# Kernel tuning notes

Hardware: AMD Instinct MI355X
Metric: run time of the kernel (lower is better)

Reference implementation:

```python
import jax, jax.numpy as jnp
import numpy as np
import math

D_MODEL = 512
NUM_CLASSES = 8
MEM_SLOTS = 64
STEPS = 4
DECAY = 0.9
TOPK = 8
SCORE_CLIP = 10.0
VOCAB = 32000
MAX_LEN = 2048
B, T = 32, 2048


def _linear_params(key, d_in, d_out):
    kw, kb = jax.random.split(key)
    W = jax.random.normal(kw, (d_in, d_out), jnp.float32) * (1.0 / math.sqrt(d_in))
    b = jnp.zeros((d_out,), jnp.float32)
    return W, b


def setup_inputs() -> dict:
    key = jax.random.key(0)
    ks = jax.random.split(key, 16)
    inp = {}
    inp["input_ids"] = jax.random.randint(ks[0], (B, T), 0, VOCAB)
    inp["attention_mask"] = jnp.ones((B, T), jnp.int32)
    inp["token_emb"] = jax.random.normal(ks[1], (VOCAB, D_MODEL), jnp.float32) * 0.02
    inp["pos_emb"] = jax.random.normal(ks[2], (MAX_LEN, D_MODEL), jnp.float32) * 0.02
    inp["memory_init"] = jax.random.normal(ks[3], (1, MEM_SLOTS, D_MODEL), jnp.float32) * 0.02
    names = ["q", "k", "v", "write", "gate", "rq", "rk", "rv"]
    for i, n in enumerate(names):
        W, b = _linear_params(ks[4 + i], D_MODEL, D_MODEL)
        inp[n + "_W"], inp[n + "_b"] = W, b
    inp["fuse_W"], inp["fuse_b"] = _linear_params(ks[12], 2 * D_MODEL, D_MODEL)
    inp["cls_W"], inp["cls_b"] = _linear_params(ks[13], D_MODEL, NUM_CLASSES)
    inp["tln_g"] = jnp.ones((D_MODEL,), jnp.float32)
    inp["tln_b"] = jnp.zeros((D_MODEL,), jnp.float32)
    inp["mln_g"] = jnp.ones((D_MODEL,), jnp.float32)
    inp["mln_b"] = jnp.zeros((D_MODEL,), jnp.float32)
    return inp


def _layer_norm(x, g, b, eps=1e-5):
    mu = jnp.mean(x, axis=-1, keepdims=True)
    var = jnp.var(x, axis=-1, keepdims=True)
    return (x - mu) * jax.lax.rsqrt(var + eps) * g + b


def _topk_softmax(scores, k):
    # scores: (B, T, S). Equivalent to scatter top-k vals into -inf then softmax:
    # softmax over the top-k entries, zeros elsewhere.
    Bb, Tt, S = scores.shape
    tv, ti = jax.lax.top_k(scores, k)           # (B,T,k)
    w = jax.nn.softmax(tv, axis=-1)
    rows = jnp.arange(Bb * Tt)[:, None]
    out = jnp.zeros((Bb * Tt, S), scores.dtype).at[rows, ti.reshape(-1, k)].set(w.reshape(-1, k))
    return out.reshape(Bb, Tt, S)


def _binding(scores, mask_f, k):
    w = _topk_softmax(jnp.clip(scores, -SCORE_CLIP, SCORE_CLIP), k)
    w = w * mask_f
    return w / jnp.maximum(jnp.sum(w, axis=-1, keepdims=True), 1e-9)


def _forward(input_ids, attention_mask, token_emb, pos_emb, memory_init,
             q_W, q_b, k_W, k_b, v_W, v_b, write_W, write_b, gate_W, gate_b,
             rq_W, rq_b, rk_W, rk_b, rv_W, rv_b, fuse_W, fuse_b,
             cls_W, cls_b, tln_g, tln_b, mln_g, mln_b):
    scale = 1.0 / math.sqrt(D_MODEL)
    tokens = token_emb[input_ids] + pos_emb[jnp.arange(input_ids.shape[1])][None]
    tokens = _layer_norm(tokens, tln_g, tln_b)  # (B,T,D)
    mask_f = attention_mask[..., None].astype(tokens.dtype)  # (B,T,1)
    memory = jnp.broadcast_to(memory_init, (input_ids.shape[0], MEM_SLOTS, D_MODEL))
    for _ in range(STEPS):
        q = tokens @ q_W + q_b
        kk = memory @ k_W + k_b
        scores = jnp.einsum("btd,bsd->bts", q, kk) * scale
        binding = _binding(scores, mask_f, TOPK)  # (B,T,S)
        v = tokens @ v_W + v_b
        write = jnp.einsum("bts,btd->bsd", binding, v)
        slot_usage = jnp.maximum(jnp.sum(binding, axis=1)[..., None], 1e-6)  # (B,S,1)
        write = (write / slot_usage) @ write_W + write_b
        write = jax.nn.sigmoid(write @ gate_W + gate_b) * write
        memory = _layer_norm(DECAY * memory + (1.0 - DECAY) * write, mln_g, mln_b)
    # read
    rq = tokens @ rq_W + rq_b
    rk = memory @ rk_W + rk_b
    rv = memory @ rv_W + rv_b
    scores = jnp.einsum("btd,bsd->bts", rq, rk) * scale
    rw = _binding(scores, mask_f, TOPK)
    context = jnp.einsum("bts,bsd->btd", rw, rv)
    fused = jnp.concatenate([tokens, context], axis=-1) @ fuse_W + fuse_b
    pooled = jnp.sum(fused * mask_f, axis=1) / jnp.maximum(jnp.sum(mask_f, axis=1), 1.0)
    return pooled @ cls_W + cls_b  # (B, C)


def reference(input_ids, attention_mask, token_emb, pos_emb, memory_init,
              q_W, q_b, k_W, k_b, v_W, v_b, write_W, write_b, gate_W, gate_b,
              rq_W, rq_b, rk_W, rk_b, rv_W, rv_b, fuse_W, fuse_b,
              cls_W, cls_b, tln_g, tln_b, mln_g, mln_b):
    return _forward(input_ids, attention_mask, token_emb, pos_emb, memory_init,
                    q_W, q_b, k_W, k_b, v_W, v_b, write_W, write_b, gate_W, gate_b,
                    rq_W, rq_b, rk_W, rk_b, rv_W, rv_b, fuse_W, fuse_b,
                    cls_W, cls_b, tln_g, tln_b, mln_g, mln_b)
```

## Files before the change

kernel.cpp:

```cpp
#include <hip/hip_runtime.h>
#include <hip/hip_bf16.h>
#include <math.h>

#define BB 32
#define TT 2048
#define DM 512
#define SS 64
#define BT (BB*TT)
#define NSTEPS 4
#define SCALE 0.044194173824159216f

typedef unsigned short u16;
typedef unsigned int u32;
typedef __attribute__((ext_vector_type(8))) short s16x8;
typedef __attribute__((ext_vector_type(4))) float f32x4;
typedef __attribute__((ext_vector_type(4))) unsigned u32x4;

__device__ __forceinline__ u16 f2b(float x){
  __hip_bfloat16 h = __float2bfloat16(x);
  return *reinterpret_cast<u16*>(&h);
}
__device__ __forceinline__ float b2f(u16 u){
  __hip_bfloat16 h;
  *reinterpret_cast<u16*>(&h) = u;
  return __bfloat162float(h);
}

static __device__ __forceinline__ float wave_reduce_sum(float v){
  #pragma unroll
  for (int off=32; off; off>>=1) v += __shfl_down(v, off);
  return v;
}

__global__ __launch_bounds__(256) void embed_ln_k(const int* __restrict__ ids,
    const float* __restrict__ temb, const float* __restrict__ pemb,
    const float* __restrict__ g, const float* __restrict__ be, u16* __restrict__ out){
  int row = blockIdx.x*4 + (threadIdx.x>>6);
  int l = threadIdx.x & 63;
  int t = row & (TT-1);
  int id = ids[row];
  const float* te = temb + (size_t)id*DM + l*8;
  const float* pe = pemb + (size_t)t*DM + l*8;
  float4 a0 = *(const float4*)te,     a1 = *(const float4*)(te+4);
  float4 p0 = *(const float4*)pe,     p1 = *(const float4*)(pe+4);
  float x[8] = {a0.x+p0.x, a0.y+p0.y, a0.z+p0.z, a0.w+p0.w,
                a1.x+p1.x, a1.y+p1.y, a1.z+p1.z, a1.w+p1.w};
  float s1 = 0.f, s2 = 0.f;
  #pragma unroll
  for (int e=0;e<8;e++){ s1 += x[e]; s2 += x[e]*x[e]; }
  #pragma unroll
  for (int off=1; off<64; off<<=1){ s1 += __shfl_xor(s1, off); s2 += __shfl_xor(s2, off); }
  float mu = s1*(1.f/DM);
  float var = s2*(1.f/DM) - mu*mu;
  float rs = rsqrtf(var + 1e-5f);
  const float* gp = g + l*8;
  const float* bp = be + l*8;
  float4 g0=*(const float4*)gp, g1=*(const float4*)(gp+4);
  float4 b0=*(const float4*)bp, b1=*(const float4*)(bp+4);
  float gg[8]={g0.x,g0.y,g0.z,g0.w,g1.x,g1.y,g1.z,g1.w};
  float bb[8]={b0.x,b0.y,b0.z,b0.w,b1.x,b1.y,b1.z,b1.w};
  s16x8 o;
  #pragma unroll
  for (int e=0;e<8;e++) o[e] = (short)f2b((x[e]-mu)*rs*gg[e] + bb[e]);
  *(s16x8*)(out + (size_t)row*DM + l*8) = o;
}

template<int EPI>
__global__ __launch_bounds__(128) void ntgemm_k(const u16* __restrict__ A,
    const u16* __restrict__ Bm, const float* __restrict__ bias,
    const u16* __restrict__ mulb, const float* __restrict__ rowv,
    const float* __restrict__ bias2, void* __restrict__ Cout, float scalep){
  int m0 = blockIdx.x*32 + (threadIdx.x>>6)*16;
  int n0 = blockIdx.y*64;
  int l = threadIdx.x & 63;
  int lr = l & 15, lk = (l>>4)*8;
  const u16* Arow = A + (size_t)(m0 + lr)*512 + lk;
  const u16* B0   = Bm + (size_t)(n0 + lr)*512 + lk;
  f32x4 acc[4] = {};
  #pragma unroll
  for (int k0=0;k0<512;k0+=32){
    s16x8 a = *(const s16x8*)(Arow + k0);
    #pragma unroll
    for (int j=0;j<4;j++){
      s16x8 b = *(const s16x8*)(B0 + (size_t)j*16*512 + k0);
      acc[j] = __builtin_amdgcn_mfma_f32_16x16x32_bf16(a, b, acc[j], 0,0,0);
    }
  }
  int mbase = m0 + (l>>4)*4;
  #pragma unroll
  for (int j=0;j<4;j++){
    int n = n0 + j*16 + lr;
    #pragma unroll
    for (int r=0;r<4;r++){
      int m = mbase + r;
      float v = acc[j][r];
      if (EPI==2){
        float z = v + bias[n];
        float sg = 1.f/(1.f + expf(-z));
        ((float*)Cout)[(size_t)m*512 + n] = b2f(mulb[(size_t)m*512 + n]) * sg;
      }
      if (EPI==3){ ((float*)Cout)[(size_t)m*512 + n] = v + bias[n]; }
      if (EPI==5){ ((u16*)Cout)[(size_t)m*512 + n] = f2b(v + rowv[m]*bias[n] + bias2[n]); }
    }
  }
}

__global__ __launch_bounds__(128) void ptcb_k(const u16* __restrict__ A,
    const u16* __restrict__ Bm, const float* __restrict__ bias,
    const float* __restrict__ mem, const float* __restrict__ wcb,
    const float* __restrict__ cb0p, u16* __restrict__ Pt, float* __restrict__ cb){
  int l = threadIdx.x & 63;
  if (blockIdx.y < 8){
    int m0 = blockIdx.x*32 + (threadIdx.x>>6)*16;
    int n0 = blockIdx.y*64;
    int lr = l & 15, lk = (l>>4)*8;
    const u16* Arow = A + (size_t)(m0 + lr)*512 + lk;
    const u16* B0   = Bm + (size_t)(n0 + lr)*512 + lk;
    f32x4 acc[4] = {};
    #pragma unroll
    for (int k0=0;k0<512;k0+=32){
      s16x8 a = *(const s16x8*)(Arow + k0);
      #pragma unroll
      for (int j=0;j<4;j++){
        s16x8 b = *(const s16x8*)(B0 + (size_t)j*16*512 + k0);
        acc[j] = __builtin_amdgcn_mfma_f32_16x16x32_bf16(a, b, acc[j], 0,0,0);
      }
    }
    int mbase = m0 + (l>>4)*4;
    #pragma unroll
    for (int j=0;j<4;j++){
      int n = n0 + j*16 + lr;
      #pragma unroll
      for (int r=0;r<4;r++)
        Pt[(size_t)(mbase+r)*512 + n] = f2b(acc[j][r] + bias[n]);
    }
  } else {
    int base = blockIdx.x*32 + (threadIdx.x>>6)*16;
    for (int i=0;i<16;i++){
      int row = base + i;
      const float* r = mem + (size_t)row*512;
      float s = 0.f;
      #pragma unroll
      for (int k=0;k<8;k++) s += r[l + 64*k]*wcb[l + 64*k];
      #pragma unroll
      for (int off=32; off; off>>=1) s += __shfl_xor(s, off);
      if (l==0) cb[row] = s + cb0p[0];
    }
  }
}

__global__ __launch_bounds__(64) void bind_k(const u16* __restrict__ tok,
    const u16* __restrict__ Pt, const float* __restrict__ cbuf, const int* __restrict__ mask,
    u16* __restrict__ BNDT, float* __restrict__ cspart){
  int b = blockIdx.y, t0 = blockIdx.x*64;
  int l = threadIdx.x;
  int lr = l&15, g = l>>4, lk = g*8;
  __shared__ float sc[64*66];
  __shared__ u16 bt[64*66];

  const u16* Abase = tok + ((size_t)(b*TT + t0 + lr))*512 + lk;
  const u16* Bbase = Pt + ((size_t)(b*SS + lr))*512 + lk;
  f32x4 acc[4][4] = {};
  #pragma unroll
  for (int k0=0;k0<512;k0+=32){
    s16x8 a[4], bb[4];
    #pragma unroll
    for (int mi=0;mi<4;mi++) a[mi] = *(const s16x8*)(Abase + (size_t)mi*16*512 + k0);
    #pragma unroll
    for (int nj=0;nj<4;nj++) bb[nj] = *(const s16x8*)(Bbase + (size_t)nj*16*512 + k0);
    #pragma unroll
    for (int mi=0;mi<4;mi++)
      #pragma unroll
      for (int nj=0;nj<4;nj++)
        acc[mi][nj] = __builtin_amdgcn_mfma_f32_16x16x32_bf16(a[mi], bb[nj], acc[mi][nj], 0,0,0);
  }
  float cbv[4];
  #pragma unroll
  for (int nj=0;nj<4;nj++) cbv[nj] = cbuf[b*SS + 16*nj + lr];
  #pragma unroll
  for (int mi=0;mi<4;mi++)
    #pragma unroll
    for (int nj=0;nj<4;nj++)
      #pragma unroll
      for (int r=0;r<4;r++){
        float x = acc[mi][nj][r] + cbv[nj];
        x = fminf(fmaxf(x, -10.f), 10.f);
        sc[(16*mi + 4*g + r)*66 + 16*nj + lr] = x;
      }

  float sv[64];
  #pragma unroll
  for (int j=0;j<64;j++) sv[j] = sc[l*66 + j];

  u32 work[64];
  #pragma unroll
  for (int j=0;j<64;j++){
    u32 s = __float_as_uint(sv[j]);
    u32 o = s ^ ((u32)(((int)s) >> 31) | 0x80000000u);
    work[j] = (o & 0xFFFFFFC0u) | (u32)(63 - j);
  }
  u32 mtop = 0;
  #pragma unroll
  for (int it=0; it<8; ++it){
    u32 a[32];
    #pragma unroll
    for (int j=0;j<32;j++){ u32 x = work[2*j], y = work[2*j+1]; a[j] = x>y?x:y; }
    #pragma unroll
    for (int lvl=16; lvl>=1; lvl>>=1)
      #pragma unroll
      for (int j=0;j<lvl;j++){ u32 x = a[2*j], y = a[2*j+1]; a[j] = x>y?x:y; }
    u32 m = a[0];
    if (it==0) mtop = m;
    #pragma unroll
    for (int j=0;j<64;j++) work[j] = (work[j]==m) ? 0u : work[j];
  }
  u32 ot = mtop & 0xFFFFFFC0u;
  u32 tb = (ot & 0x80000000u) ? (ot ^ 0x80000000u) : ~ot;
  float T = __uint_as_float(tb);

  float tot = 0.f;
  #pragma unroll
  for (int j=0;j<64;j++){
    float ej = (work[j]==0u) ? expf(sv[j]-T) : 0.f;
    sv[j] = ej;
    tot += ej;
  }
  int mv = mask[b*TT + t0 + l];
  float inv = mv ? 1.f/tot : 0.f;
  #pragma unroll
  for (int j=0;j<64;j++)
    bt[j*66 + l] = f2b(sv[j]*inv);

  const u32* btw = (const u32*)bt;
  u32 rowbuf[32];
  float csum = 0.f;
  #pragma unroll
  for (int w=0;w<32;w++){
    u32 v = btw[l*33 + w];
    rowbuf[w] = v;
    csum += b2f((u16)(v & 0xFFFFu)) + b2f((u16)(v >> 16));
  }
  cspart[((size_t)b*32 + blockIdx.x)*64 + l] = csum;
  u16* dst = BNDT + ((size_t)(b*SS + l))*TT + t0;
  #pragma unroll
  for (int w8=0;w8<8;w8++){
    u32x4 v;
    v[0]=rowbuf[4*w8]; v[1]=rowbuf[4*w8+1]; v[2]=rowbuf[4*w8+2]; v[3]=rowbuf[4*w8+3];
    *(u32x4*)(dst + 8*w8) = v;
  }
}

__global__ __launch_bounds__(64) void csred_k(const float* __restrict__ cspart,
    float* __restrict__ slot, float* __restrict__ rr, float* __restrict__ raw){
  int b = blockIdx.x, s = threadIdx.x;
  float t = 0.f;
  for (int k=0;k<32;k++) t += cspart[((size_t)b*32 + k)*64 + s];
  raw[b*SS+s] = t;
  float sl = fmaxf(t, 1e-6f);
  slot[b*SS+s] = sl;
  rr[b*SS+s] = t/sl;
}

__global__ __launch_bounds__(256) void wtfused_k(const u16* __restrict__ BNDT,
    const u16* __restrict__ tok, const float* __restrict__ slot, u16* __restrict__ t1h){
  int dgrp = blockIdx.x, b = blockIdx.y;
  int tid = threadIdx.x, w = tid>>6, l = tid&63;
  int lr = l&15, lk = (l>>4)*8;
  __shared__ u16 tk[64][72];
  f32x4 acc[4] = {};
  int trow = tid>>2, dcol = (tid&3)*16;
  const u16* tokbase = tok + ((size_t)b*TT)*512 + dgrp*64;
  const u16* Abase = BNDT + ((size_t)(b*SS + 16*w + lr))*TT;
  for (int tb=0; tb<TT; tb+=64){
    const u16* src = tokbase + (size_t)(tb + trow)*512 + dcol;
    s16x8 v0 = *(const s16x8*)(src);
    s16x8 v1 = *(const s16x8*)(src+8);
    #pragma unroll
    for (int e=0;e<8;e++){
      int d0 = dcol+e, d1 = dcol+8+e;
      tk[d0][(trow + 8*((d0>>5)&1)) & 63] = (u16)v0[e];
      tk[d1][(trow + 8*((d1>>5)&1)) & 63] = (u16)v1[e];
    }
    __syncthreads();
    #pragma unroll
    for (int kst=0;kst<2;kst++){
      s16x8 a = *(const s16x8*)(Abase + tb + kst*32 + lk);
      #pragma unroll
      for (int nt=0;nt<4;nt++){
        int dd = nt*16 + lr;
        int cb2 = (kst*32 + lk + 8*((dd>>5)&1)) & 63;
        s16x8 bb = *(const s16x8*)&tk[dd][cb2];
        acc[nt] = __builtin_amdgcn_mfma_f32_16x16x32_bf16(a, bb, acc[nt], 0,0,0);
      }
    }
    __syncthreads();
  }
  #pragma unroll
  for (int nt=0;nt<4;nt++){
    int d = dgrp*64 + nt*16 + lr;
    #pragma unroll
    for (int r=0;r<4;r++){
      int s = 16*w + (l>>4)*4 + r;
      int row = b*64 + s;
      t1h[(size_t)row*512 + d] = f2b(acc[nt][r] / slot[row]);
    }
  }
}

__global__ __launch_bounds__(256) void allconv_k(
    const float* __restrict__ s0, u16* __restrict__ d0,
    const float* __restrict__ s1, u16* __restrict__ d1,
    const float* __restrict__ s2, u16* __restrict__ d2,
    const float* __restrict__ s3, u16* __restrict__ d3,
    const float* __restrict__ s4, u16* __restrict__ d4){
  int sel = blockIdx.x >> 10;
  int i = (blockIdx.x & 1023)*256 + threadIdx.x;
  const float* s; u16* d;
  if (sel==0){s=s0;d=d0;} else if (sel==1){s=s1;d=d1;} else if (sel==2){s=s2;d=d2;}
  else if (sel==3){s=s3;d=d3;} else {s=s4;d=d4;}
  d[i] = f2b(s[i]);
}

__global__ __launch_bounds__(256) void alltconv_k(
    const float* __restrict__ s0, u16* __restrict__ d0,
    const float* __restrict__ s1, u16* __restrict__ d1,
    const float* __restrict__ s2, u16* __restrict__ d2){
  const float* in; u16* out;
  if (blockIdx.z==0){in=s0;out=d0;} else if (blockIdx.z==1){in=s1;out=d1;} else {in=s2;out=d2;}
  __shared__ float t[32][33];
  int c0 = blockIdx.x*32, r0 = blockIdx.y*32;
  int cx = threadIdx.x&31, ry = threadIdx.x>>5;
  #pragma unroll
  for (int i=0;i<4;i++){ int r = ry + i*8; t[r][cx] = in[(size_t)(r0+r)*512 + c0+cx]; }
  __syncthreads();
  #pragma unroll
  for (int i=0;i<4;i++){ int r = ry + i*8; out[(size_t)(c0+r)*512 + r0+cx] = f2b(t[cx][r]); }
}

__global__ __launch_bounds__(128) void pregemm_k(
    const u16* __restrict__ A0, const u16* __restrict__ B0, u16* __restrict__ C0, float p0,
    const u16* __restrict__ A1, const u16* __restrict__ B1, u16* __restrict__ C1, float p1,
    const u16* __restrict__ A2, const u16* __restrict__ B2, u16* __restrict__ C2, float p2){
  const u16* A; const u16* Bm; u16* C; float sp;
  if (blockIdx.z==0){A=A0;Bm=B0;C=C0;sp=p0;}
  else if (blockIdx.z==1){A=A1;Bm=B1;C=C1;sp=p1;}
  else {A=A2;Bm=B2;C=C2;sp=p2;}
  int m0 = blockIdx.x*32 + (threadIdx.x>>6)*16;
  int n0 = blockIdx.y*64;
  int l = threadIdx.x & 63;
  int lr = l & 15, lk = (l>>4)*8;
  const u16* Arow = A + (size_t)(m0 + lr)*512 + lk;
  const u16* Bp   = Bm + (size_t)(n0 + lr)*512 + lk;
  f32x4 acc[4] = {};
  #pragma unroll
  for (int k0=0;k0<512;k0+=32){
    s16x8 a = *(const s16x8*)(Arow + k0);
    #pragma unroll
    for (int j=0;j<4;j++){
      s16x8 b = *(const s16x8*)(Bp + (size_t)j*16*512 + k0);
      acc[j] = __builtin_amdgcn_mfma_f32_16x16x32_bf16(a, b, acc[j], 0,0,0);
    }
  }
  int mbase = m0 + (l>>4)*4;
  #pragma unroll
  for (int j=0;j<4;j++){
    int n = n0 + j*16 + lr;
    #pragma unroll
    for (int r=0;r<4;r++)
      C[(size_t)(mbase+r)*512 + n] = f2b(acc[j][r] * sp);
  }
}

__global__ __launch_bounds__(256) void smalls_k(
    const float* __restrict__ qW, const float* __restrict__ kB, float* __restrict__ bq,
    const float* __restrict__ rqW, const float* __restrict__ rkB, float* __restrict__ bq_r,
    const float* __restrict__ kW, const float* __restrict__ qB, float* __restrict__ wcb,
    const float* __restrict__ rkW, const float* __restrict__ rqB, float* __restrict__ wcb_r,
    const float* __restrict__ wrW, const float* __restrict__ vB, float* __restrict__ bvw,
    float* __restrict__ cb0s){
  int blk = blockIdx.x;
  if (blk < 512){
    int which = blk >> 7;
    const float* W; const float* v; float* out;
    if (which==0){W=qW; v=kB; out=bq;}
    else if (which==1){W=rqW; v=rkB; out=bq_r;}
    else if (which==2){W=kW; v=qB; out=wcb;}
    else {W=rkW; v=rqB; out=wcb_r;}
    int i = (blk&127)*4 + (threadIdx.x>>6), l = threadIdx.x&63;
    const float* r = W + (size_t)i*512;
    float s = 0.f;
    #pragma unroll
    for (int k=0;k<8;k++) s += r[l + 64*k]*v[l + 64*k];
    #pragma unroll
    for (int off=32; off; off>>=1) s += __shfl_xor(s, off);
    if (l==0) out[i] = s * SCALE;
  } else if (blk < 514){
    int n = (blk-512)*256 + threadIdx.x;
    float s = 0.f;
    for (int o=0;o<512;o++) s += vB[o]*wrW[(size_t)o*512 + n];
    bvw[n] = s;
  } else {
    if (threadIdx.x < 128){
      int w = threadIdx.x>>6, l = threadIdx.x&63;
      const float* a = w ? rkB : kB;
      const float* bvec = w ? rqB : qB;
      float s = 0.f;
      #pragma unroll
      for (int k=0;k<8;k++) s += a[l + 64*k]*bvec[l + 64*k];
      #pragma unroll
      for (int off=32; off; off>>=1) s += __shfl_xor(s, off);
      if (l==0) cb0s[w] = s * SCALE;
    }
  }
}

__global__ __launch_bounds__(256) void meminit_k(const float* __restrict__ src,
    float* __restrict__ mem, u16* __restrict__ memh){
  int i = blockIdx.x*256 + threadIdx.x;
  float v = src[i & (SS*DM-1)];
  mem[i] = v;
  memh[i] = f2b(v);
}

__global__ __launch_bounds__(256) void mem_ln_k(float* __restrict__ mem, const float* __restrict__ w3,
    const float* __restrict__ g, const float* __restrict__ be, u16* __restrict__ memh){
  int row = blockIdx.x;
  int d = threadIdx.x;
  float* mrow = mem + (size_t)row*DM;
  const float* wrow = w3 + (size_t)row*DM;
  float x0 = 0.9f*mrow[d]     + 0.1f*wrow[d];
  float x1 = 0.9f*mrow[d+256] + 0.1f*wrow[d+256];
  float s1 = x0+x1, s2 = x0*x0 + x1*x1;
  s1 = wave_reduce_sum(s1); s2 = wave_reduce_sum(s2);
  __shared__ float r1[4], r2[4];
  int lane = d & 63, w = d>>6;
  if (lane==0){ r1[w]=s1; r2[w]=s2; }
  __syncthreads();
  float S1 = r1[0]+r1[1]+r1[2]+r1[3];
  float S2 = r2[0]+r2[1]+r2[2]+r2[3];
  float mu = S1 * (1.f/DM);
  float var = S2*(1.f/DM) - mu*mu;
  float rs = rsqrtf(var + 1e-5f);
  float y0 = (x0-mu)*rs*g[d] + be[d];
  float y1 = (x1-mu)*rs*g[d+256] + be[d+256];
  mrow[d] = y0; mrow[d+256] = y1;
  memh[(size_t)row*DM + d] = f2b(y0);
  memh[(size_t)row*DM + d+256] = f2b(y1);
}

__global__ __launch_bounds__(256) void tokpart_k(const u16* __restrict__ tok,
    const int* __restrict__ mask, float* __restrict__ tp){
  int b = blockIdx.x, sl = blockIdx.y;
  int w = threadIdx.x>>6, l = threadIdx.x&63;
  float acc[8] = {};
  #pragma unroll 4
  for (int i=0;i<32;i++){
    int t = sl*128 + w + 4*i;
    float m = (float)mask[b*TT + t];
    s16x8 v = *(const s16x8*)(tok + ((size_t)(b*TT + t))*512 + l*8);
    #pragma unroll
    for (int e=0;e<8;e++) acc[e] += m*b2f((u16)v[e]);
  }
  float* dst = tp + ((size_t)(b*64 + sl*4 + w))*512 + l*8;
  #pragma unroll
  for (int e=0;e<8;e++) dst[e] = acc[e];
}

__global__ __launch_bounds__(256) void catden_k(const float* __restrict__ tp,
    const float* __restrict__ rws, const float* __restrict__ rv,
    const int* __restrict__ mask, float* __restrict__ cat, float* __restrict__ denomv){
  int b = blockIdx.x, tid = threadIdx.x;
  float dn = 0.f;
  for (int t=tid; t<TT; t+=256) dn += (float)mask[b*TT+t];
  dn = wave_reduce_sum(dn);
  __shared__ float dred[4];
  if ((tid&63)==0) dred[tid>>6]=dn;
  #pragma unroll
  for (int it=0; it<2; ++it){
    int d = tid + it*256;
    float ts = 0.f;
    for (int k=0;k<64;k++) ts += tp[((size_t)(b*64+k))*512 + d];
    cat[(size_t)b*1024 + d] = ts;
    float c = 0.f;
    for (int s=0;s<SS;s++) c += rws[b*SS+s]*rv[((size_t)b*SS+s)*DM + d];
    cat[(size_t)b*1024 + 512 + d] = c;
  }
  __syncthreads();
  if (tid==0) denomv[b] = dred[0]+dred[1]+dred[2]+dred[3];
}

__global__ __launch_bounds__(256) void fuse_k(const float* __restrict__ cat,
    const float* __restrict__ denomv, const float* __restrict__ fuseW,
    const float* __restrict__ fuseb, float* __restrict__ pooled){
  int b = blockIdx.x, n0 = blockIdx.y*64;
  int l = threadIdx.x&63, kc = threadIdx.x>>6;
  int n = n0 + l;
  float acc = 0.f;
  const float* crow = cat + (size_t)b*1024;
  for (int k=kc*256; k<kc*256+256; ++k)
    acc += crow[k]*fuseW[(size_t)k*512 + n];
  __shared__ float red[4][64];
  red[kc][l] = acc;
  __syncthreads();
  if (kc==0){
    float denom = denomv[b];
    float tot = red[0][l]+red[1][l]+red[2][l]+red[3][l];
    pooled[(size_t)b*512 + n] = (tot + denom*fuseb[n]) / fmaxf(denom, 1.f);
  }
}

__global__ __launch_bounds__(256) void cls_k(const float* __restrict__ pooled,
    const float* __restrict__ clsW, const float* __restrict__ clsb, float* __restrict__ out){
  int b = blockIdx.x;
  int c = threadIdx.x&7, kc = threadIdx.x>>3;
  float acc = 0.f;
  const float* prow = pooled + (size_t)b*512;
  for (int d=kc*16; d<kc*16+16; ++d) acc += prow[d]*clsW[d*8+c];
  __shared__ float red[32][8];
  red[kc][c] = acc;
  __syncthreads();
  if (threadIdx.x < 8){
    float tot = 0.f;
    #pragma unroll
    for (int k=0;k<32;k++) tot += red[k][threadIdx.x];
    out[b*8 + threadIdx.x] = tot + clsb[threadIdx.x];
  }
}

extern "C" void kernel_launch(void* const* d_in, const int* in_sizes, int n_in,
                              void* d_out, int out_size, void* d_ws, size_t ws_size,
                              hipStream_t stream){
  (void)in_sizes; (void)n_in; (void)out_size; (void)ws_size;
  const int*   ids   = (const int*)d_in[0];
  const int*   amask = (const int*)d_in[1];
  const float* temb  = (const float*)d_in[2];
  const float* pemb  = (const float*)d_in[3];
  const float* mem0  = (const float*)d_in[4];
  const float* qW=(const float*)d_in[5],  *qB=(const float*)d_in[6];
  const float* kW=(const float*)d_in[7],  *kB=(const float*)d_in[8];
  const float* vW=(const float*)d_in[9],  *vB=(const float*)d_in[10];
  const float* wrW=(const float*)d_in[11],*wrB=(const float*)d_in[12];
  const float* gtW=(const float*)d_in[13],*gtB=(const float*)d_in[14];
  const float* rqW=(const float*)d_in[15],*rqB=(const float*)d_in[16];
  const float* rkW=(const float*)d_in[17],*rkB=(const float*)d_in[18];
  const float* rvW=(const float*)d_in[19],*rvB=(const float*)d_in[20];
  const float* fW=(const float*)d_in[21], *fB=(const float*)d_in[22];
  const float* cW=(const float*)d_in[23], *cB=(const float*)d_in[24];
  const float* tg=(const float*)d_in[25], *tb=(const float*)d_in[26];
  const float* mg=(const float*)d_in[27], *mb=(const float*)d_in[28];

  char* p = (char*)d_ws;
  size_t off = 0;
  auto alloc = [&](size_t bytes)->char*{ char* r = p + off; off += (bytes + 255) & ~(size_t)255; return r; };
  u16*   tokens = (u16*)  alloc((size_t)BT*DM*2);
  u16*   Pt     = (u16*)  alloc((size_t)BB*SS*DM*2);
  u16*   BNDT   = (u16*)  alloc((size_t)BB*SS*TT*2);
  float* cspart = (float*)alloc((size_t)BB*32*64*4);
  float* scratch= (float*)alloc((size_t)4*2048*512*4);
  u16*   t1h    = (u16*)  alloc((size_t)2048*512*2);
  u16*   zh     = (u16*)  alloc((size_t)2048*512*2);
  float* mem    = (float*)alloc((size_t)BB*SS*DM*4);
  u16*   memh   = (u16*)  alloc((size_t)BB*SS*DM*2);
  u16*   wrWT   = (u16*)  alloc(512*512*2);
  u16*   gtWT   = (u16*)  alloc(512*512*2);
  u16*   rvWT   = (u16*)  alloc(512*512*2);
  u16*   WqkT   = (u16*)  alloc(512*512*2);
  u16*   WqkT_r = (u16*)  alloc(512*512*2);
  u16*   WvwT   = (u16*)  alloc(512*512*2);
  float* bq     = (float*)alloc(512*4);
  float* bq_r   = (float*)alloc(512*4);
  float* wcb    = (float*)alloc(512*4);
  float* wcb_r  = (float*)alloc(512*4);
  float* bvw    = (float*)alloc(512*4);
  float* cb0s   = (float*)alloc(256);
  float* cbuf   = (float*)alloc(2048*4);
  float* slot   = (float*)alloc(2048*4);
  float* rr     = (float*)alloc(2048*4);
  float* raw    = (float*)alloc(2048*4);
  float* catbuf = (float*)alloc((size_t)BB*1024*4);
  float* denomv = (float*)alloc(BB*4);
  float* pooled = (float*)alloc((size_t)BB*512*4);
  float* rv32   = scratch;
  float* tspart = scratch + 1048576;
  float* gh32   = scratch + 2097152;
  u16*   qWb    = (u16*)((char*)scratch + 12582912);
  u16*   kWb    = qWb + 512*512;
  u16*   rqWb   = kWb + 512*512;
  u16*   rkWb   = rqWb + 512*512;
  u16*   vWb    = (u16*)((char*)scratch + 14680064);

  allconv_k<<<5120, 256, 0, stream>>>(qW, qWb, kW, kWb, rqW, rqWb, rkW, rkWb, vW, vWb);
  alltconv_k<<<dim3(16,16,3), 256, 0, stream>>>(wrW, wrWT, gtW, gtWT, rvW, rvWT);
  pregemm_k<<<dim3(16,8,3), 128, 0, stream>>>(qWb, kWb, WqkT, SCALE,
                                              rqWb, rkWb, WqkT_r, SCALE,
                                              wrWT, vWb, WvwT, 1.0f);
  smalls_k<<<515, 256, 0, stream>>>(qW, kB, bq, rqW, rkB, bq_r, kW, qB, wcb,
                                    rkW, rqB, wcb_r, wrW, vB, bvw, cb0s);
  embed_ln_k<<<BT/4, 256, 0, stream>>>(ids, temb, pemb, tg, tb, tokens);
  meminit_k<<<(BB*SS*DM)/256, 256, 0, stream>>>(mem0, mem, memh);

  for (int step=0; step<NSTEPS; ++step){
    ptcb_k<<<dim3(64,9), 128, 0, stream>>>(memh, WqkT, bq, mem, wcb, cb0s, Pt, cbuf);
    bind_k<<<dim3(32,32), 64, 0, stream>>>(tokens, Pt, cbuf, amask, BNDT, cspart);
    csred_k<<<32, 64, 0, stream>>>(cspart, slot, rr, raw);
    wtfused_k<<<dim3(8,32), 256, 0, stream>>>(BNDT, tokens, slot, t1h);
    ntgemm_k<5><<<dim3(64,8), 128, 0, stream>>>(t1h, WvwT, bvw, nullptr, rr, wrB, zh, 0.f);
    ntgemm_k<2><<<dim3(64,8), 128, 0, stream>>>(zh, gtWT, gtB, zh, nullptr, nullptr, gh32, 0.f);
    mem_ln_k<<<BB*SS, 256, 0, stream>>>(mem, gh32, mg, mb, memh);
  }

  ptcb_k<<<dim3(64,9), 128, 0, stream>>>(memh, WqkT_r, bq_r, mem, wcb_r, cb0s+1, Pt, cbuf);
  bind_k<<<dim3(32,32), 64, 0, stream>>>(tokens, Pt, cbuf, amask, BNDT, cspart);
  csred_k<<<32, 64, 0, stream>>>(cspart, slot, rr, raw);
  ntgemm_k<3><<<dim3(64,8), 128, 0, stream>>>(memh, rvWT, rvB, nullptr, nullptr, nullptr, rv32, 0.f);
  tokpart_k<<<dim3(32,16), 256, 0, stream>>>(tokens, amask, tspart);
  catden_k<<<32, 256, 0, stream>>>(tspart, raw, rv32, amask, catbuf, denomv);
  fuse_k<<<dim3(32,8), 256, 0, stream>>>(catbuf, denomv, fW, fB, pooled);
  cls_k<<<32, 256, 0, stream>>>(pooled, cW, cB, (float*)d_out);
}
```

Measured before the change: 624.5 us.

## Split-K the binding-weighted token GEMM and process two rows per wave in embed LN

The memory-write GEMM (binding^T × tokens) is split along T into 4 partitions, each block covering 128 output columns. Partial fp32 sums go to a scratch buffer, and a separate reduction kernel adds them and applies the slot normalization. This raises the block count from 256 to 512 and halves the token reads per output column, which helps occupancy on a GPU with many CUs. The cost is extra fp32 partial-sum traffic and one more launch per step. Separately, embed_ln now handles two rows per wave to raise memory-level parallelism.

```diff
diff --git a/kernel.cpp b/kernel.cpp
--- a/kernel.cpp
+++ b/kernel.cpp
@@ -35,34 +35,48 @@
 __global__ __launch_bounds__(256) void embed_ln_k(const int* __restrict__ ids,
     const float* __restrict__ temb, const float* __restrict__ pemb,
     const float* __restrict__ g, const float* __restrict__ be, u16* __restrict__ out){
-  int row = blockIdx.x*4 + (threadIdx.x>>6);
-  int l = threadIdx.x & 63;
-  int t = row & (TT-1);
-  int id = ids[row];
-  const float* te = temb + (size_t)id*DM + l*8;
-  const float* pe = pemb + (size_t)t*DM + l*8;
-  float4 a0 = *(const float4*)te,     a1 = *(const float4*)(te+4);
-  float4 p0 = *(const float4*)pe,     p1 = *(const float4*)(pe+4);
-  float x[8] = {a0.x+p0.x, a0.y+p0.y, a0.z+p0.z, a0.w+p0.w,
-                a1.x+p1.x, a1.y+p1.y, a1.z+p1.z, a1.w+p1.w};
-  float s1 = 0.f, s2 = 0.f;
-  #pragma unroll
-  for (int e=0;e<8;e++){ s1 += x[e]; s2 += x[e]*x[e]; }
-  #pragma unroll
-  for (int off=1; off<64; off<<=1){ s1 += __shfl_xor(s1, off); s2 += __shfl_xor(s2, off); }
-  float mu = s1*(1.f/DM);
-  float var = s2*(1.f/DM) - mu*mu;
-  float rs = rsqrtf(var + 1e-5f);
+  int w = threadIdx.x>>6, l = threadIdx.x & 63;
+  int row0 = blockIdx.x*8 + w*2;
+  int row1 = row0 + 1;
+  int t0 = row0 & (TT-1), t1 = row1 & (TT-1);
+  int id0 = ids[row0], id1 = ids[row1];
+  const float* teA = temb + (size_t)id0*DM + l*8;
+  const float* peA = pemb + (size_t)t0*DM + l*8;
+  const float* teB = temb + (size_t)id1*DM + l*8;
+  const float* peB = pemb + (size_t)t1*DM + l*8;
+  float4 a0=*(const float4*)teA, a1=*(const float4*)(teA+4);
+  float4 c0=*(const float4*)teB, c1=*(const float4*)(teB+4);
+  float4 p0=*(const float4*)peA, p1=*(const float4*)(peA+4);
+  float4 q0=*(const float4*)peB, q1=*(const float4*)(peB+4);
+  float xA[8] = {a0.x+p0.x, a0.y+p0.y, a0.z+p0.z, a0.w+p0.w,
+                 a1.x+p1.x, a1.y+p1.y, a1.z+p1.z, a1.w+p1.w};
+  float xB[8] = {c0.x+q0.x, c0.y+q0.y, c0.z+q0.z, c0.w+q0.w,
+                 c1.x+q1.x, c1.y+q1.y, c1.z+q1.z, c1.w+q1.w};
+  float sA1=0.f, sA2=0.f, sB1=0.f, sB2=0.f;
+  #pragma unroll
+  for (int e=0;e<8;e++){ sA1 += xA[e]; sA2 += xA[e]*xA[e]; sB1 += xB[e]; sB2 += xB[e]*xB[e]; }
+  #pragma unroll
+  for (int off=1; off<64; off<<=1){
+    sA1 += __shfl_xor(sA1, off); sA2 += __shfl_xor(sA2, off);
+    sB1 += __shfl_xor(sB1, off); sB2 += __shfl_xor(sB2, off);
+  }
+  float muA = sA1*(1.f/DM), muB = sB1*(1.f/DM);
+  float rsA = rsqrtf(sA2*(1.f/DM) - muA*muA + 1e-5f);
+  float rsB = rsqrtf(sB2*(1.f/DM) - muB*muB + 1e-5f);
   const float* gp = g + l*8;
   const float* bp = be + l*8;
   float4 g0=*(const float4*)gp, g1=*(const float4*)(gp+4);
   float4 b0=*(const float4*)bp, b1=*(const float4*)(bp+4);
   float gg[8]={g0.x,g0.y,g0.z,g0.w,g1.x,g1.y,g1.z,g1.w};
   float bb[8]={b0.x,b0.y,b0.z,b0.w,b1.x,b1.y,b1.z,b1.w};
-  s16x8 o;
-  #pragma unroll
-  for (int e=0;e<8;e++) o[e] = (short)f2b((x[e]-mu)*rs*gg[e] + bb[e]);
-  *(s16x8*)(out + (size_t)row*DM + l*8) = o;
+  s16x8 oA, oB;
+  #pragma unroll
+  for (int e=0;e<8;e++){
+    oA[e] = (short)f2b((xA[e]-muA)*rsA*gg[e] + bb[e]);
+    oB[e] = (short)f2b((xB[e]-muB)*rsB*gg[e] + bb[e]);
+  }
+  *(s16x8*)(out + (size_t)row0*DM + l*8) = oA;
+  *(s16x8*)(out + (size_t)row1*DM + l*8) = oB;
 }
 
 template<int EPI>
@@ -261,50 +275,63 @@
   rr[b*SS+s] = t/sl;
 }
 
-__global__ __launch_bounds__(256) void wtfused_k(const u16* __restrict__ BNDT,
-    const u16* __restrict__ tok, const float* __restrict__ slot, u16* __restrict__ t1h){
-  int dgrp = blockIdx.x, b = blockIdx.y;
+__global__ __launch_bounds__(256) void wt_k(const u16* __restrict__ BNDT,
+    const u16* __restrict__ tok, float* __restrict__ part){
+  int dgrp = blockIdx.x, b = blockIdx.y, ks = blockIdx.z;
   int tid = threadIdx.x, w = tid>>6, l = tid&63;
   int lr = l&15, lk = (l>>4)*8;
-  __shared__ u16 tk[64][72];
-  f32x4 acc[4] = {};
-  int trow = tid>>2, dcol = (tid&3)*16;
-  const u16* tokbase = tok + ((size_t)b*TT)*512 + dgrp*64;
+  __shared__ u16 tk[128][72];
+  f32x4 acc[8] = {};
+  int trow = tid>>2, dseg = (tid&3)*32;
+  const u16* tokbase = tok + ((size_t)b*TT)*512 + dgrp*128;
   const u16* Abase = BNDT + ((size_t)(b*SS + 16*w + lr))*TT;
-  for (int tb=0; tb<TT; tb+=64){
-    const u16* src = tokbase + (size_t)(tb + trow)*512 + dcol;
+  for (int chunk=0; chunk<8; ++chunk){
+    int tb = ks*512 + chunk*64;
+    const u16* src = tokbase + (size_t)(tb + trow)*512 + dseg;
     s16x8 v0 = *(const s16x8*)(src);
     s16x8 v1 = *(const s16x8*)(src+8);
+    s16x8 v2 = *(const s16x8*)(src+16);
+    s16x8 v3 = *(const s16x8*)(src+24);
     #pragma unroll
     for (int e=0;e<8;e++){
-      int d0 = dcol+e, d1 = dcol+8+e;
-      tk[d0][(trow + 8*((d0>>5)&1)) & 63] = (u16)v0[e];
-      tk[d1][(trow + 8*((d1>>5)&1)) & 63] = (u16)v1[e];
+      int d0 = dseg+e, d1 = dseg+8+e, d2 = dseg+16+e, d3 = dseg+24+e;
+      tk[d0][(trow + 8*((d0>>5)&3)) & 63] = (u16)v0[e];
+      tk[d1][(trow + 8*((d1>>5)&3)) & 63] = (u16)v1[e];
+      tk[d2][(trow + 8*((d2>>5)&3)) & 63] = (u16)v2[e];
+      tk[d3][(trow + 8*((d3>>5)&3)) & 63] = (u16)v3[e];
     }
     __syncthreads();
     #pragma unroll
     for (int kst=0;kst<2;kst++){
       s16x8 a = *(const s16x8*)(Abase + tb + kst*32 + lk);
       #pragma unroll
-      for (int nt=0;nt<4;nt++){
+      for (int nt=0;nt<8;nt++){
         int dd = nt*16 + lr;
-        int cb2 = (kst*32 + lk + 8*((dd>>5)&1)) & 63;
+        int cb2 = (kst*32 + lk + 8*((dd>>5)&3)) & 63;
         s16x8 bb = *(const s16x8*)&tk[dd][cb2];
         acc[nt] = __builtin_amdgcn_mfma_f32_16x16x32_bf16(a, bb, acc[nt], 0,0,0);
       }
     }
     __syncthreads();
   }
-  #pragma unroll
-  for (int nt=0;nt<4;nt++){
-    int d = dgrp*64 + nt*16 + lr;
+  float* dst = part + (size_t)ks*2048*512 + ((size_t)(b*SS))*512 + dgrp*128;
+  #pragma unroll
+  for (int nt=0;nt<8;nt++){
+    int d = nt*16 + lr;
     #pragma unroll
     for (int r=0;r<4;r++){
       int s = 16*w + (l>>4)*4 + r;
-      int row = b*64 + s;
-      t1h[(size_t)row*512 + d] = f2b(acc[nt][r] / slot[row]);
-    }
-  }
+      dst[(size_t)s*512 + d] = acc[nt][r];
+    }
+  }
+}
+
+__global__ __launch_bounds__(256) void wtred_k(const float* __restrict__ part,
+    const float* __restrict__ slot, u16* __restrict__ t1h){
+  int i = blockIdx.x*256 + threadIdx.x;
+  int row = i>>9;
+  float v = part[i] + part[i + 2048*512] + part[i + 2*2048*512] + part[i + 3*2048*512];
+  t1h[i] = f2b(v / slot[row]);
 }
 
 __global__ __launch_bounds__(256) void allconv_k(
@@ -556,7 +583,7 @@
   u16*   Pt     = (u16*)  alloc((size_t)BB*SS*DM*2);
   u16*   BNDT   = (u16*)  alloc((size_t)BB*SS*TT*2);
   float* cspart = (float*)alloc((size_t)BB*32*64*4);
-  float* scratch= (float*)alloc((size_t)4*2048*512*4);
+  float* wtpart = (float*)alloc((size_t)4*2048*512*4);
   u16*   t1h    = (u16*)  alloc((size_t)2048*512*2);
   u16*   zh     = (u16*)  alloc((size_t)2048*512*2);
   float* mem    = (float*)alloc((size_t)BB*SS*DM*4);
@@ -580,14 +607,14 @@
   float* catbuf = (float*)alloc((size_t)BB*1024*4);
   float* denomv = (float*)alloc(BB*4);
   float* pooled = (float*)alloc((size_t)BB*512*4);
-  float* rv32   = scratch;
-  float* tspart = scratch + 1048576;
-  float* gh32   = scratch + 2097152;
-  u16*   qWb    = (u16*)((char*)scratch + 12582912);
+  float* rv32   = wtpart;
+  float* tspart = wtpart + 1048576;
+  float* gh32   = wtpart + 2097152;
+  u16*   qWb    = (u16*)((char*)wtpart + 12582912);
   u16*   kWb    = qWb + 512*512;
   u16*   rqWb   = kWb + 512*512;
   u16*   rkWb   = rqWb + 512*512;
-  u16*   vWb    = (u16*)((char*)scratch + 14680064);
+  u16*   vWb    = (u16*)((char*)wtpart + 14680064);
 
   allconv_k<<<5120, 256, 0, stream>>>(qW, qWb, kW, kWb, rqW, rqWb, rkW, rkWb, vW, vWb);
   alltconv_k<<<dim3(16,16,3), 256, 0, stream>>>(wrW, wrWT, gtW, gtWT, rvW, rvWT);
@@ -596,14 +623,15 @@
                                               wrWT, vWb, WvwT, 1.0f);
   smalls_k<<<515, 256, 0, stream>>>(qW, kB, bq, rqW, rkB, bq_r, kW, qB, wcb,
                                     rkW, rqB, wcb_r, wrW, vB, bvw, cb0s);
-  embed_ln_k<<<BT/4, 256, 0, stream>>>(ids, temb, pemb, tg, tb, tokens);
+  embed_ln_k<<<BT/8, 256, 0, stream>>>(ids, temb, pemb, tg, tb, tokens);
   meminit_k<<<(BB*SS*DM)/256, 256, 0, stream>>>(mem0, mem, memh);
 
   for (int step=0; step<NSTEPS; ++step){
     ptcb_k<<<dim3(64,9), 128, 0, stream>>>(memh, WqkT, bq, mem, wcb, cb0s, Pt, cbuf);
     bind_k<<<dim3(32,32), 64, 0, stream>>>(tokens, Pt, cbuf, amask, BNDT, cspart);
     csred_k<<<32, 64, 0, stream>>>(cspart, slot, rr, raw);
-    wtfused_k<<<dim3(8,32), 256, 0, stream>>>(BNDT, tokens, slot, t1h);
+    wt_k<<<dim3(4,32,4), 256, 0, stream>>>(BNDT, tokens, wtpart);
+    wtred_k<<<4096, 256, 0, stream>>>(wtpart, slot, t1h);
     ntgemm_k<5><<<dim3(64,8), 128, 0, stream>>>(t1h, WvwT, bvw, nullptr, rr, wrB, zh, 0.f);
     ntgemm_k<2><<<dim3(64,8), 128, 0, stream>>>(zh, gtWT, gtB, zh, nullptr, nullptr, gh32, 0.f);
     mem_ln_k<<<BB*SS, 256, 0, stream>>>(mem, gh32, mg, mb, memh);
```

Result: faster. 569.7 us (-8.8%).
